# Performance work log

Measured on AMD Instinct MI355X. Metric: run time of the kernel, lower is better.

Reference implementation:

```python
import jax, jax.numpy as jnp
import numpy as np

D_MODEL = 96
D_INNER = 2 * D_MODEL          # expand=2
D_STATE = 16
D_CONV = 4
DT_RANK = 6                    # ceil(96/16)


def setup_inputs() -> dict:
    key = jax.random.key(0)
    ks = jax.random.split(key, 12)
    B, C, H, W = 4, D_MODEL, 64, 64
    # dt_proj bias init (inverse-softplus of dt sampled log-uniform in [1e-3, 1e-1])
    dtv = jnp.exp(jax.random.uniform(ks[7], (D_INNER,), jnp.float32)
                  * (np.log(0.1) - np.log(0.001)) + np.log(0.001))
    dtv = jnp.clip(dtv, 1e-4, None)
    dt_proj_b = dtv + jnp.log(-jnp.expm1(-dtv))
    dt_std = DT_RANK ** -0.5
    return {
        "x": jax.random.normal(ks[0], (B, C, H, W), jnp.float32),
        "proj_w": jax.random.normal(ks[1], (2 * C, C, 1, 1), jnp.float32) * 0.05,
        "dconv_w": jax.random.normal(ks[2], (C, 2 * C, 3, 3), jnp.float32) * 0.02,
        "in_proj_w": jax.random.normal(ks[3], (2 * D_INNER, C), jnp.float32) * 0.05,
        "conv1d_w": jax.random.normal(ks[4], (D_INNER, D_CONV), jnp.float32) * 0.2,
        "conv1d_b": jnp.zeros((D_INNER,), jnp.float32),
        "x_proj_w": jax.random.normal(ks[5], (DT_RANK + 2 * D_STATE, D_INNER), jnp.float32) * 0.05,
        "dt_proj_w": jax.random.uniform(ks[6], (D_INNER, DT_RANK), jnp.float32, -dt_std, dt_std),
        "dt_proj_b": dt_proj_b,
        "A_log": jnp.log(jnp.tile(jnp.arange(1, D_STATE + 1, dtype=jnp.float32), (D_INNER, 1))),
        "D": jnp.ones((D_INNER,), jnp.float32),
        "out_proj_w": jax.random.normal(ks[8], (C, D_INNER), jnp.float32) * 0.05,
    }


def _cssm_forward(x, proj_w, dconv_w, in_proj_w, conv1d_w, conv1d_b,
                  x_proj_w, dt_proj_w, dt_proj_b, A_log, D, out_proj_w):
    Bsz, Cdim, H, W = x.shape
    L = H * W
    # proj (1x1 conv, no bias) then dconv (3x3 conv, pad 1, no bias)
    xp = jax.lax.conv_general_dilated(x, proj_w, (1, 1), 'VALID',
                                      dimension_numbers=('NCHW', 'OIHW', 'NCHW'))
    xp = jax.lax.conv_general_dilated(xp, dconv_w, (1, 1), ((1, 1), (1, 1)),
                                      dimension_numbers=('NCHW', 'OIHW', 'NCHW'))
    seq = xp.reshape(Bsz, Cdim, L).transpose(0, 2, 1)            # (B, L, C)
    # in_proj (no bias) -> (B, 2*d_inner, L)
    xz = jnp.einsum('blc,ec->bel', seq, in_proj_w)
    xin, z = jnp.split(xz, 2, axis=1)                             # (B, d_inner, L) each
    # causal depthwise conv1d (pad d_conv-1 on left) + SiLU
    xpad = jnp.pad(xin, ((0, 0), (0, 0), (D_CONV - 1, 0)))
    xc = jax.lax.conv_general_dilated(xpad, conv1d_w[:, None, :], (1,), 'VALID',
                                      dimension_numbers=('NCH', 'OIH', 'NCH'),
                                      feature_group_count=D_INNER)
    xc = jax.nn.silu(xc + conv1d_b[None, :, None])                # (B, d_inner, L)
    # x_proj -> dt (rank), B (state), C (state)
    x_dbl = jnp.einsum('bdl,ed->ble', xc, x_proj_w)               # (B, L, rank+2n)
    dt, Bc, Cc = jnp.split(x_dbl, [DT_RANK, DT_RANK + D_STATE], axis=-1)
    delta = jax.nn.softplus(jnp.einsum('blr,dr->bld', dt, dt_proj_w) + dt_proj_b)  # (B,L,d)
    A = -jnp.exp(A_log)                                           # (d, n)
    u = xc.transpose(0, 2, 1)                                     # (B, L, d)
    # selective scan: h_t = exp(delta_t A) * h_{t-1} + delta_t B_t u_t  (diag, per channel/state)
    dA = jnp.exp(delta[..., None] * A)                            # (B,L,d,n)
    dBu = delta[..., None] * Bc[:, :, None, :] * u[..., None]     # (B,L,d,n)

    def combine(c1, c2):
        a1, b1 = c1
        a2, b2 = c2
        return a2 * a1, a2 * b1 + b2

    _, h = jax.lax.associative_scan(combine, (dA, dBu), axis=1)   # (B,L,d,n)
    y = jnp.einsum('bldn,bln->bld', h, Cc) + D * u                # (B,L,d)
    y = y * jax.nn.silu(z.transpose(0, 2, 1))                     # gate
    out = jnp.einsum('bld,cd->blc', y, out_proj_w)                # (B,L,C)
    return out.transpose(0, 2, 1).reshape(Bsz, Cdim, H, W)


def reference(x, proj_w, dconv_w, in_proj_w, conv1d_w, conv1d_b,
              x_proj_w, dt_proj_w, dt_proj_b, A_log, D, out_proj_w):
    return _cssm_forward(x, proj_w, dconv_w, in_proj_w, conv1d_w, conv1d_b,
                         x_proj_w, dt_proj_w, dt_proj_b, A_log, D, out_proj_w)
```

## Files before the change

### kernel.cpp

```cpp
#include <hip/hip_runtime.h>
#include <math.h>

#define LL    4096
#define CDIM  96
#define DIN   192
#define NST   16
#define XE    38

typedef __attribute__((ext_vector_type(8))) short v8s;
typedef __attribute__((ext_vector_type(4))) float v4f;
typedef unsigned short ushort_t;
typedef unsigned int uint_t;

#if __has_builtin(__builtin_amdgcn_exp2f)
__device__ __forceinline__ float fexp2(float x) { return __builtin_amdgcn_exp2f(x); }
#else
__device__ __forceinline__ float fexp2(float x) { return exp2f(x); }
#endif
#if __has_builtin(__builtin_amdgcn_logf)
__device__ __forceinline__ float flog2(float x) { return __builtin_amdgcn_logf(x); }
#else
__device__ __forceinline__ float flog2(float x) { return __log2f(x); }
#endif

__device__ __forceinline__ float siluf(float x) {
    return x * __builtin_amdgcn_rcpf(1.f + fexp2(-1.44269504f * x));
}
__device__ __forceinline__ ushort_t f2bf(float f) {
    uint_t u = __builtin_bit_cast(uint_t, f);
    return (ushort_t)((u + 0x7fffu + ((u >> 16) & 1u)) >> 16);
}
__device__ __forceinline__ float bf2f(ushort_t u) {
    return __builtin_bit_cast(float, (uint_t)u << 16);
}

__global__ __launch_bounds__(256) void k_prep(const float* __restrict__ proj_w,
                                              const float* __restrict__ dconv_w,
                                              const float* __restrict__ in_proj_w,
                                              const float* __restrict__ out_proj_w,
                                              const float* __restrict__ x_proj_w,
                                              const float* __restrict__ x,
                                              ushort_t* __restrict__ Wbf,
                                              ushort_t* __restrict__ Wibf,
                                              ushort_t* __restrict__ Wobf,
                                              ushort_t* __restrict__ Wxbf,
                                              ushort_t* __restrict__ xT) {
    int bid = blockIdx.x;
    if (bid < 576) {
        int i = bid * 256 + threadIdx.x;
        if (i < 82944) {
            int k = i % 9;
            int c = (i / 9) % 96;
            int o = i / 864;
            float s = 0.f;
            for (int j = 0; j < 192; ++j)
                s += dconv_w[(o * 192 + j) * 9 + k] * proj_w[j * 96 + c];
            Wbf[(k * 96 + o) * 96 + c] = f2bf(s);
            return;
        }
        i -= 82944;
        if (i < 36864) { Wibf[i] = f2bf(in_proj_w[i]); return; }
        i -= 36864;
        if (i < 18432) { Wobf[i] = f2bf(out_proj_w[i]); return; }
        i -= 18432;
        if (i < 9216) {
            int e = i / 192;
            Wxbf[i] = (e < XE) ? f2bf(x_proj_w[i]) : (ushort_t)0;
        }
        return;
    }
    int bid2 = bid - 576;
    int yy = bid2 % 66;
    int b  = bid2 / 66;
    int yv = yy - 1;
    for (int i = threadIdx.x; i < 68 * 12; i += 256) {
        int xx = i % 68, cig = i / 68;
        int xv = xx - 1;
        ushort_t u[8];
        if (yv >= 0 && yv < 64 && xv >= 0 && xv < 64) {
            const float* sp = x + ((size_t)(b * 96 + cig * 8)) * LL + yv * 64 + xv;
#pragma unroll
            for (int j = 0; j < 8; ++j) u[j] = f2bf(sp[j * LL]);
        } else {
#pragma unroll
            for (int j = 0; j < 8; ++j) u[j] = 0;
        }
        uint4 pk;
        pk.x = u[0] | ((uint_t)u[1] << 16); pk.y = u[2] | ((uint_t)u[3] << 16);
        pk.z = u[4] | ((uint_t)u[5] << 16); pk.w = u[6] | ((uint_t)u[7] << 16);
        *(uint4*)(xT + (((size_t)b * 66 + yy) * 68 + xx) * 96 + cig * 8) = pk;
    }
}

__global__ __launch_bounds__(384, 2) void k_convin(const ushort_t* __restrict__ xT,
                                                   const ushort_t* __restrict__ Wbf,
                                                   const ushort_t* __restrict__ Wibf,
                                                   ushort_t* __restrict__ xzb) {
    __shared__ ushort_t s_seq[32 * 104];
    int tid = threadIdx.x;
    int w = tid >> 6, l = tid & 63;
    int n = l & 15, g = l >> 4;
    int blk = blockIdx.x;
    int b = blk >> 7, rem = blk & 127;
    int y = rem >> 1, half = rem & 1;
    int lx = (w & 1) * 16;
    int x0 = half * 32 + lx;
    int co0 = (w >> 1) * 32;
    v4f acc0 = {0.f, 0.f, 0.f, 0.f};
    v4f acc1 = {0.f, 0.f, 0.f, 0.f};
    const ushort_t* xb = xT + (((size_t)b * 66 + y) * 68 + x0 + n) * 96 + g * 8;
    const ushort_t* aw = Wbf + ((size_t)co0 + n) * 96 + g * 8;
#pragma unroll
    for (int tap = 0; tap < 9; ++tap) {
        int dy = tap / 3, dx = tap % 3;
        const ushort_t* bp = xb + (dy * 68 + dx) * 96;
        const ushort_t* ap = aw + (size_t)tap * 9216;
#pragma unroll
        for (int kk = 0; kk < 3; ++kk) {
            v8s bf = *(const v8s*)(bp + kk * 32);
            v8s a0 = *(const v8s*)(ap + kk * 32);
            v8s a1 = *(const v8s*)(ap + 1536 + kk * 32);
            acc0 = __builtin_amdgcn_mfma_f32_16x16x32_bf16(a0, bf, acc0, 0, 0, 0);
            acc1 = __builtin_amdgcn_mfma_f32_16x16x32_bf16(a1, bf, acc1, 0, 0, 0);
        }
    }
    {
        int ll = lx + n;
        ushort_t* sp = s_seq + ll * 104 + co0 + g * 4;
        ushort4 p0, p1;
        p0.x = f2bf(acc0[0]); p0.y = f2bf(acc0[1]); p0.z = f2bf(acc0[2]); p0.w = f2bf(acc0[3]);
        p1.x = f2bf(acc1[0]); p1.y = f2bf(acc1[1]); p1.z = f2bf(acc1[2]); p1.w = f2bf(acc1[3]);
        *(ushort4*)sp = p0;
        *(ushort4*)(sp + 16) = p1;
    }
    __syncthreads();
    int coh = w * 64;
    v4f acc[4][2];
#pragma unroll
    for (int mt = 0; mt < 4; ++mt)
#pragma unroll
        for (int lt = 0; lt < 2; ++lt) acc[mt][lt] = (v4f){0.f, 0.f, 0.f, 0.f};
    const ushort_t* ap2 = Wibf + ((size_t)coh + n) * 96 + g * 8;
#pragma unroll
    for (int lt = 0; lt < 2; ++lt) {
        const ushort_t* bp2 = s_seq + (lt * 16 + n) * 104 + g * 8;
#pragma unroll
        for (int kk = 0; kk < 3; ++kk) {
            v8s bf = *(const v8s*)(bp2 + kk * 32);
#pragma unroll
            for (int mt = 0; mt < 4; ++mt) {
                v8s af = *(const v8s*)(ap2 + mt * 16 * 96 + kk * 32);
                acc[mt][lt] = __builtin_amdgcn_mfma_f32_16x16x32_bf16(af, bf, acc[mt][lt], 0, 0, 0);
            }
        }
    }
    int l0g = y * 64 + half * 32;
    ushort_t* ob = xzb + (size_t)b * 384 * LL + l0g + n;
#pragma unroll
    for (int mt = 0; mt < 4; ++mt) {
        int e = coh + mt * 16 + g * 4;
#pragma unroll
        for (int lt = 0; lt < 2; ++lt)
#pragma unroll
            for (int r = 0; r < 4; ++r)
                ob[(size_t)(e + r) * LL + lt * 16] = f2bf(acc[mt][lt][r]);
    }
}

__global__ __launch_bounds__(256) void k_conv1d(const ushort_t* __restrict__ xzb,
                                                const float* __restrict__ w,
                                                const float* __restrict__ bias,
                                                float* __restrict__ xc,
                                                ushort_t* __restrict__ xcT) {
    int tid = threadIdx.x;
    int d_l = tid >> 2, tg = tid & 3;
    int b = blockIdx.z, dg = blockIdx.y, tt = blockIdx.x;
    int d = dg * 64 + d_l;
    int t0 = tt * 16 + tg * 4;
    const ushort_t* xin = xzb + (size_t)(b * 384 + d) * LL;
    ushort4 cu = *(const ushort4*)(xin + t0);
    float pm3 = 0.f, pm2 = 0.f, pm1 = 0.f;
    if (t0 > 0) {
        ushort4 pv = *(const ushort4*)(xin + t0 - 4);
        pm3 = bf2f(pv.y); pm2 = bf2f(pv.z); pm1 = bf2f(pv.w);
    }
    float in[7] = {pm3, pm2, pm1, bf2f(cu.x), bf2f(cu.y), bf2f(cu.z), bf2f(cu.w)};
    float w0 = w[d * 4 + 0], w1 = w[d * 4 + 1], w2 = w[d * 4 + 2], w3 = w[d * 4 + 3];
    float bb = bias[d];
    float o[4];
#pragma unroll
    for (int i = 0; i < 4; ++i) {
        float s = bb + w0 * in[i] + w1 * in[i + 1] + w2 * in[i + 2] + w3 * in[i + 3];
        o[i] = siluf(s);
    }
    float4 ov; ov.x = o[0]; ov.y = o[1]; ov.z = o[2]; ov.w = o[3];
    *(float4*)(xc + (size_t)(b * DIN + d) * LL + t0) = ov;
    ushort_t* xt = xcT + ((size_t)b * 4096 + t0) * DIN + d;
#pragma unroll
    for (int i = 0; i < 4; ++i)
        xt[(size_t)i * DIN] = f2bf(o[i]);
}

__global__ __launch_bounds__(256, 4) void k_xprojm(const ushort_t* __restrict__ xcT,
                                                   const ushort_t* __restrict__ Wxbf,
                                                   float* __restrict__ dtT,
                                                   float* __restrict__ BtP,
                                                   float* __restrict__ CtP) {
    int tid = threadIdx.x;
    int w = tid >> 6, l = tid & 63;
    int n = l & 15, g = l >> 4;
    int b = blockIdx.y;
    int l0 = blockIdx.x * 64 + w * 16;
    const ushort_t* bp = xcT + ((size_t)b * 4096 + l0 + n) * 192 + g * 8;
    const ushort_t* ap = Wxbf + (size_t)n * 192 + g * 8;
    v4f acc[3];
#pragma unroll
    for (int m = 0; m < 3; ++m) acc[m] = (v4f){0.f, 0.f, 0.f, 0.f};
#pragma unroll
    for (int kk = 0; kk < 6; ++kk) {
        v8s bf = *(const v8s*)(bp + kk * 32);
#pragma unroll
        for (int m = 0; m < 3; ++m) {
            v8s af = *(const v8s*)(ap + m * 16 * 192 + kk * 32);
            acc[m] = __builtin_amdgcn_mfma_f32_16x16x32_bf16(af, bf, acc[m], 0, 0, 0);
        }
    }
    float* dtb = dtT + (size_t)b * 6 * LL + l0 + n;
    float* Bb = BtP + ((size_t)b * LL + l0 + n) * 16;
    float* Cb = CtP + ((size_t)b * LL + l0 + n) * 16;
#pragma unroll
    for (int m = 0; m < 3; ++m)
#pragma unroll
        for (int r = 0; r < 4; ++r) {
            int e = m * 16 + g * 4 + r;
            float v = acc[m][r];
            if (e < 6)       dtb[(size_t)e * LL] = v;
            else if (e < 22) Bb[e - 6] = v;
            else if (e < 38) Cb[e - 22] = v;
        }
}

__global__ __launch_bounds__(512, 6) void k_scan(const float* __restrict__ dtT,
                                                 const float* __restrict__ dtw,
                                                 const float* __restrict__ dtpb,
                                                 const float* __restrict__ xc,
                                                 const float* __restrict__ BtP,
                                                 const float* __restrict__ CtP,
                                                 const float* __restrict__ A_log,
                                                 const float* __restrict__ Dp,
                                                 ushort_t* __restrict__ xzb) {
    __shared__ float s_d[32 * 132];
    __shared__ float s_u[32 * 132];
    __shared__ float s_a[32][17];
    __shared__ float s_h[32][17];
    int tid = threadIdx.x;
    int n = tid & 15, cg = tid >> 4;
    int bd = blockIdx.x;
    int d = bd % DIN, b = bd / DIN;
    const float* urow = xc + (size_t)(b * DIN + d) * LL;
    const ushort_t* zrow = xzb + (size_t)(b * 384 + DIN + d) * LL;
    ushort_t* ygr = xzb + (size_t)(b * 384 + d) * LL;
    float A2 = -__expf(A_log[d * NST + n]) * 1.44269504f;
    float Dd = Dp[d];

    {
        int t8 = tid * 8;
        int li = ((t8 >> 7) * 132) + (t8 & 127);
        const float* dt0 = dtT + (size_t)b * 6 * LL + t8;
        v4f ra[6], rb[6];
#pragma unroll
        for (int r = 0; r < 6; ++r) {
            ra[r] = *(const v4f*)(dt0 + r * LL);
            rb[r] = *(const v4f*)(dt0 + r * LL + 4);
        }
        const float* wr = dtw + d * 6;
        float w0 = wr[0], w1 = wr[1], w2 = wr[2], w3 = wr[3], w4 = wr[4], w5 = wr[5];
        float bb = dtpb[d];
        v4f spa, spb;
#pragma unroll
        for (int j = 0; j < 4; ++j) {
            float s1 = bb + w0 * ra[0][j] + w1 * ra[1][j] + w2 * ra[2][j]
                          + w3 * ra[3][j] + w4 * ra[4][j] + w5 * ra[5][j];
            spa[j] = 0.69314718f * flog2(1.f + fexp2(s1 * 1.44269504f));
            float s2 = bb + w0 * rb[0][j] + w1 * rb[1][j] + w2 * rb[2][j]
                          + w3 * rb[3][j] + w4 * rb[4][j] + w5 * rb[5][j];
            spb[j] = 0.69314718f * flog2(1.f + fexp2(s2 * 1.44269504f));
        }
        *(v4f*)&s_d[li]     = spa;
        *(v4f*)&s_d[li + 4] = spb;
        *(float4*)&s_u[li]     = *(const float4*)(urow + t8);
        *(float4*)&s_u[li + 4] = *(const float4*)(urow + t8 + 4);
    }
    __syncthreads();

    int t0 = cg * 128;
    int lb = cg * 132;
    const float* pB = BtP + ((size_t)b * LL + t0) * 16 + n;
    const float* pC = CtP + ((size_t)b * LL + t0) * 16 + n;

    float h = 0.f, sdu = 0.f;
    float4 du_c = *(float4*)&s_d[lb];
    float4 u_c  = *(float4*)&s_u[lb];
    float B0 = pB[0], B1 = pB[16], B2 = pB[32], B3 = pB[48];
    for (int s = 0; s < 31; ++s) {
        int ln = lb + s * 4 + 4;
        const float* pBn = pB + s * 64 + 64;
        float4 du_n = *(float4*)&s_d[ln];
        float4 u_n  = *(float4*)&s_u[ln];
        float Bn0 = pBn[0], Bn1 = pBn[16], Bn2 = pBn[32], Bn3 = pBn[48];
        float a0 = fexp2(du_c.x * A2), a1 = fexp2(du_c.y * A2);
        float a2 = fexp2(du_c.z * A2), a3 = fexp2(du_c.w * A2);
        h = fmaf(a0, h, (du_c.x * u_c.x) * B0);
        h = fmaf(a1, h, (du_c.y * u_c.y) * B1);
        h = fmaf(a2, h, (du_c.z * u_c.z) * B2);
        h = fmaf(a3, h, (du_c.w * u_c.w) * B3);
        sdu += (du_c.x + du_c.y) + (du_c.z + du_c.w);
        du_c = du_n; u_c = u_n; B0 = Bn0; B1 = Bn1; B2 = Bn2; B3 = Bn3;
    }
    {
        float a0 = fexp2(du_c.x * A2), a1 = fexp2(du_c.y * A2);
        float a2 = fexp2(du_c.z * A2), a3 = fexp2(du_c.w * A2);
        h = fmaf(a0, h, (du_c.x * u_c.x) * B0);
        h = fmaf(a1, h, (du_c.y * u_c.y) * B1);
        h = fmaf(a2, h, (du_c.z * u_c.z) * B2);
        h = fmaf(a3, h, (du_c.w * u_c.w) * B3);
        sdu += (du_c.x + du_c.y) + (du_c.z + du_c.w);
    }
    s_a[cg][n] = fexp2(sdu * A2);
    s_h[cg][n] = h;
    __syncthreads();

    {
        int l = tid & 63, w = tid >> 6;
        int c = l & 31, nn = (w << 1) | (l >> 5);
        float a  = s_a[c][nn];
        float hh = s_h[c][nn];
#pragma unroll
        for (int st = 1; st < 32; st <<= 1) {
            float ap = __shfl_up(a, st, 32);
            float hp = __shfl_up(hh, st, 32);
            bool ok = (c >= st);
            hh = ok ? fmaf(a, hp, hh) : hh;
            a  = ok ? a * ap : a;
        }
        float h0 = __shfl_up(hh, 1, 32);
        if (c == 0) h0 = 0.f;
        s_a[c][nn] = h0;
    }
    __syncthreads();

    h = s_a[cg][n];
    const int j = n & 3;
    const bool e1 = (j == 1), e2 = (j == 2), e3 = (j == 3);
    du_c = *(float4*)&s_d[lb];
    u_c  = *(float4*)&s_u[lb];
    B0 = pB[0]; B1 = pB[16]; B2 = pB[32]; B3 = pB[48];
    float C0 = pC[0], C1 = pC[16], C2 = pC[32], C3 = pC[48];
    ushort4 z_c = *(const ushort4*)(zrow + t0);
    for (int s = 0; s < 32; ++s) {
        float4 du_n, u_n;
        ushort4 z_n;
        float Bn0, Bn1, Bn2, Bn3, Cn0, Cn1, Cn2, Cn3;
        if (s < 31) {
            int ln = lb + s * 4 + 4;
            const float* pBn = pB + s * 64 + 64;
            const float* pCn = pC + s * 64 + 64;
            du_n = *(float4*)&s_d[ln];
            u_n  = *(float4*)&s_u[ln];
            Bn0 = pBn[0]; Bn1 = pBn[16]; Bn2 = pBn[32]; Bn3 = pBn[48];
            Cn0 = pCn[0]; Cn1 = pCn[16]; Cn2 = pCn[32]; Cn3 = pCn[48];
            z_n = *(const ushort4*)(zrow + t0 + s * 4 + 4);
        }
        float a0 = fexp2(du_c.x * A2), a1 = fexp2(du_c.y * A2);
        float a2 = fexp2(du_c.z * A2), a3 = fexp2(du_c.w * A2);
        h = fmaf(a0, h, (du_c.x * u_c.x) * B0); float p0 = h * C0;
        h = fmaf(a1, h, (du_c.y * u_c.y) * B1); float p1 = h * C1;
        h = fmaf(a2, h, (du_c.z * u_c.z) * B2); float p2 = h * C2;
        h = fmaf(a3, h, (du_c.w * u_c.w) * B3); float p3 = h * C3;
        p0 += __shfl_xor(p0, 1); p0 += __shfl_xor(p0, 2);
        p1 += __shfl_xor(p1, 1); p1 += __shfl_xor(p1, 2);
        p2 += __shfl_xor(p2, 1); p2 += __shfl_xor(p2, 2);
        p3 += __shfl_xor(p3, 1); p3 += __shfl_xor(p3, 2);
        float pj = e3 ? p3 : (e2 ? p2 : (e1 ? p1 : p0));
        pj += __shfl_xor(pj, 4); pj += __shfl_xor(pj, 8);
        float uj = e3 ? u_c.w : (e2 ? u_c.z : (e1 ? u_c.y : u_c.x));
        ushort_t zu = e3 ? z_c.w : (e2 ? z_c.z : (e1 ? z_c.y : z_c.x));
        float yj = fmaf(Dd, uj, pj) * siluf(bf2f(zu));
        if (n < 4)
            ygr[t0 + s * 4 + n] = f2bf(yj);
        du_c = du_n; u_c = u_n; z_c = z_n;
        B0 = Bn0; B1 = Bn1; B2 = Bn2; B3 = Bn3;
        C0 = Cn0; C1 = Cn1; C2 = Cn2; C3 = Cn3;
    }
}

__global__ __launch_bounds__(512, 2) void k_outproj(const ushort_t* __restrict__ xzb,
                                                    const ushort_t* __restrict__ Wobf,
                                                    float* __restrict__ out) {
    __shared__ ushort_t s_yg[64][216];
    int tid = threadIdx.x;
    int b = blockIdx.y;
    int l0 = blockIdx.x * 64;
    const ushort_t* ygb = xzb + (size_t)b * 384 * LL;
    {
        int q = tid & 63, o = tid >> 6;
        if (q < 48) {
            uint4 v[4];
#pragma unroll
            for (int jj = 0; jj < 4; ++jj)
                v[jj] = *(const uint4*)(ygb + (size_t)(q * 4 + jj) * LL + l0 + o * 8);
            const ushort_t* vs = (const ushort_t*)v;
#pragma unroll
            for (int j2 = 0; j2 < 8; ++j2) {
                ushort4 pk;
                pk.x = vs[j2]; pk.y = vs[8 + j2]; pk.z = vs[16 + j2]; pk.w = vs[24 + j2];
                *(ushort4*)&s_yg[o * 8 + j2][q * 4] = pk;
            }
        }
    }
    __syncthreads();
    int w = tid >> 6, l = tid & 63;
    int n = l & 15, g = l >> 4;
    int lt = (w >> 1) * 16;
    int c0 = (w & 1) * 48;
    const ushort_t* bp = &s_yg[lt + n][g * 8];
    const ushort_t* ap = Wobf + ((size_t)c0 + n) * 192 + g * 8;
    v4f acc[3];
#pragma unroll
    for (int m = 0; m < 3; ++m) acc[m] = (v4f){0.f, 0.f, 0.f, 0.f};
#pragma unroll
    for (int kk = 0; kk < 6; ++kk) {
        v8s bf = *(const v8s*)(bp + kk * 32);
#pragma unroll
        for (int m = 0; m < 3; ++m) {
            v8s af = *(const v8s*)(ap + m * 16 * 192 + kk * 32);
            acc[m] = __builtin_amdgcn_mfma_f32_16x16x32_bf16(af, bf, acc[m], 0, 0, 0);
        }
    }
    float* ob = out + (size_t)b * 96 * LL + l0 + lt + n;
#pragma unroll
    for (int m = 0; m < 3; ++m)
#pragma unroll
        for (int r = 0; r < 4; ++r)
            ob[(size_t)(c0 + m * 16 + g * 4 + r) * LL] = acc[m][r];
}

extern "C" void kernel_launch(void* const* d_in, const int* in_sizes, int n_in,
                              void* d_out, int out_size, void* d_ws, size_t ws_size,
                              hipStream_t stream) {
    const float* x         = (const float*)d_in[0];
    const float* proj_w    = (const float*)d_in[1];
    const float* dconv_w   = (const float*)d_in[2];
    const float* in_proj_w = (const float*)d_in[3];
    const float* conv1d_w  = (const float*)d_in[4];
    const float* conv1d_b  = (const float*)d_in[5];
    const float* x_proj_w  = (const float*)d_in[6];
    const float* dt_proj_w = (const float*)d_in[7];
    const float* dt_proj_b = (const float*)d_in[8];
    const float* A_log     = (const float*)d_in[9];
    const float* Dp        = (const float*)d_in[10];
    const float* out_proj_w= (const float*)d_in[11];
    float* out = (float*)d_out;
    float* ws  = (float*)d_ws;

    ushort_t* Wbf  = (ushort_t*)ws;
    ushort_t* Wibf = (ushort_t*)(ws + 41472);
    ushort_t* Wobf = (ushort_t*)(ws + 59904);
    ushort_t* Wxbf = (ushort_t*)(ws + 69120);
    ushort_t* xT   = (ushort_t*)(ws + 73728);
    ushort_t* xzb  = (ushort_t*)(ws + 1721856);
    float* xc   = ws + 4867584;
    float* dtT  = xc + 3145728;
    float* BtP  = dtT + 98304;
    float* CtP  = BtP + 262144;
    ushort_t* xcT = (ushort_t*)(CtP + 262144);

    k_prep<<<dim3(840), dim3(256), 0, stream>>>(proj_w, dconv_w, in_proj_w, out_proj_w,
                                                x_proj_w, x, Wbf, Wibf, Wobf, Wxbf, xT);
    k_convin<<<dim3(512), dim3(384), 0, stream>>>(xT, Wbf, Wibf, xzb);
    k_conv1d<<<dim3(256, 3, 4), dim3(256), 0, stream>>>(xzb, conv1d_w, conv1d_b, xc, xcT);
    k_xprojm<<<dim3(64, 4), dim3(256), 0, stream>>>(xcT, Wxbf, dtT, BtP, CtP);
    k_scan<<<dim3(768), dim3(512), 0, stream>>>(dtT, dt_proj_w, dt_proj_b, xc, BtP, CtP,
                                                A_log, Dp, xzb);
    k_outproj<<<dim3(64, 4), dim3(512), 0, stream>>>(xzb, Wobf, out);
}
```

Measured before the change: 114.9 us.

## Recompute conv1d in scan instead of storing fp32 xc; retile outproj

Drops the fp32 xc buffer that conv1d wrote and the scan read back. The scan now recomputes the depthwise conv1d plus SiLU from the bf16 xin rows, which removes a 12MB write and read of global memory in exchange for a small amount of extra arithmetic. The out-projection kernel is also retiled to 16-position blocks with 384 threads, one MFMA tile per wave, giving more blocks and higher occupancy. The dt load in the scan is split into two halves to lower register pressure.

Result: no change. 115.9 us (+0.9%).

```diff
diff --git a/kernel.cpp b/kernel.cpp
--- a/kernel.cpp
+++ b/kernel.cpp
@@ -170,7 +170,6 @@
 __global__ __launch_bounds__(256) void k_conv1d(const ushort_t* __restrict__ xzb,
                                                 const float* __restrict__ w,
                                                 const float* __restrict__ bias,
-                                                float* __restrict__ xc,
                                                 ushort_t* __restrict__ xcT) {
     int tid = threadIdx.x;
     int d_l = tid >> 2, tg = tid & 3;
@@ -187,18 +186,12 @@
     float in[7] = {pm3, pm2, pm1, bf2f(cu.x), bf2f(cu.y), bf2f(cu.z), bf2f(cu.w)};
     float w0 = w[d * 4 + 0], w1 = w[d * 4 + 1], w2 = w[d * 4 + 2], w3 = w[d * 4 + 3];
     float bb = bias[d];
-    float o[4];
+    ushort_t* xt = xcT + ((size_t)b * 4096 + t0) * DIN + d;
 #pragma unroll
     for (int i = 0; i < 4; ++i) {
         float s = bb + w0 * in[i] + w1 * in[i + 1] + w2 * in[i + 2] + w3 * in[i + 3];
-        o[i] = siluf(s);
-    }
-    float4 ov; ov.x = o[0]; ov.y = o[1]; ov.z = o[2]; ov.w = o[3];
-    *(float4*)(xc + (size_t)(b * DIN + d) * LL + t0) = ov;
-    ushort_t* xt = xcT + ((size_t)b * 4096 + t0) * DIN + d;
-#pragma unroll
-    for (int i = 0; i < 4; ++i)
-        xt[(size_t)i * DIN] = f2bf(o[i]);
+        xt[(size_t)i * DIN] = f2bf(siluf(s));
+    }
 }
 
 __global__ __launch_bounds__(256, 4) void k_xprojm(const ushort_t* __restrict__ xcT,
@@ -243,7 +236,8 @@
 __global__ __launch_bounds__(512, 6) void k_scan(const float* __restrict__ dtT,
                                                  const float* __restrict__ dtw,
                                                  const float* __restrict__ dtpb,
-                                                 const float* __restrict__ xc,
+                                                 const float* __restrict__ c1w,
+                                                 const float* __restrict__ c1b,
                                                  const float* __restrict__ BtP,
                                                  const float* __restrict__ CtP,
                                                  const float* __restrict__ A_log,
@@ -257,7 +251,7 @@
     int n = tid & 15, cg = tid >> 4;
     int bd = blockIdx.x;
     int d = bd % DIN, b = bd / DIN;
-    const float* urow = xc + (size_t)(b * DIN + d) * LL;
+    const ushort_t* xin  = xzb + (size_t)(b * 384 + d) * LL;
     const ushort_t* zrow = xzb + (size_t)(b * 384 + DIN + d) * LL;
     ushort_t* ygr = xzb + (size_t)(b * 384 + d) * LL;
     float A2 = -__expf(A_log[d * NST + n]) * 1.44269504f;
@@ -266,30 +260,53 @@
     {
         int t8 = tid * 8;
         int li = ((t8 >> 7) * 132) + (t8 & 127);
+        float ee[11];
+        if (t8 > 0) {
+            ushort4 pv = *(const ushort4*)(xin + t8 - 4);
+            ee[0] = bf2f(pv.y); ee[1] = bf2f(pv.z); ee[2] = bf2f(pv.w);
+        } else {
+            ee[0] = ee[1] = ee[2] = 0.f;
+        }
+        v8s cu = *(const v8s*)(xin + t8);
+#pragma unroll
+        for (int j = 0; j < 8; ++j) ee[3 + j] = bf2f((ushort_t)cu[j]);
+        float cw0 = c1w[d * 4], cw1 = c1w[d * 4 + 1], cw2 = c1w[d * 4 + 2], cw3 = c1w[d * 4 + 3];
+        float cb = c1b[d];
+#pragma unroll
+        for (int j = 0; j < 8; ++j) {
+            float s = cb + cw0 * ee[j] + cw1 * ee[j + 1] + cw2 * ee[j + 2] + cw3 * ee[j + 3];
+            s_u[li + j] = siluf(s);
+        }
         const float* dt0 = dtT + (size_t)b * 6 * LL + t8;
-        v4f ra[6], rb[6];
-#pragma unroll
-        for (int r = 0; r < 6; ++r) {
-            ra[r] = *(const v4f*)(dt0 + r * LL);
-            rb[r] = *(const v4f*)(dt0 + r * LL + 4);
-        }
         const float* wr = dtw + d * 6;
         float w0 = wr[0], w1 = wr[1], w2 = wr[2], w3 = wr[3], w4 = wr[4], w5 = wr[5];
         float bb = dtpb[d];
-        v4f spa, spb;
-#pragma unroll
-        for (int j = 0; j < 4; ++j) {
-            float s1 = bb + w0 * ra[0][j] + w1 * ra[1][j] + w2 * ra[2][j]
-                          + w3 * ra[3][j] + w4 * ra[4][j] + w5 * ra[5][j];
-            spa[j] = 0.69314718f * flog2(1.f + fexp2(s1 * 1.44269504f));
-            float s2 = bb + w0 * rb[0][j] + w1 * rb[1][j] + w2 * rb[2][j]
-                          + w3 * rb[3][j] + w4 * rb[4][j] + w5 * rb[5][j];
-            spb[j] = 0.69314718f * flog2(1.f + fexp2(s2 * 1.44269504f));
-        }
-        *(v4f*)&s_d[li]     = spa;
-        *(v4f*)&s_d[li + 4] = spb;
-        *(float4*)&s_u[li]     = *(const float4*)(urow + t8);
-        *(float4*)&s_u[li + 4] = *(const float4*)(urow + t8 + 4);
+        {
+            v4f ra[6];
+#pragma unroll
+            for (int r = 0; r < 6; ++r) ra[r] = *(const v4f*)(dt0 + r * LL);
+            v4f spa;
+#pragma unroll
+            for (int j = 0; j < 4; ++j) {
+                float s1 = bb + w0 * ra[0][j] + w1 * ra[1][j] + w2 * ra[2][j]
+                              + w3 * ra[3][j] + w4 * ra[4][j] + w5 * ra[5][j];
+                spa[j] = 0.69314718f * flog2(1.f + fexp2(s1 * 1.44269504f));
+            }
+            *(v4f*)&s_d[li] = spa;
+        }
+        {
+            v4f rb[6];
+#pragma unroll
+            for (int r = 0; r < 6; ++r) rb[r] = *(const v4f*)(dt0 + r * LL + 4);
+            v4f spb;
+#pragma unroll
+            for (int j = 0; j < 4; ++j) {
+                float s2 = bb + w0 * rb[0][j] + w1 * rb[1][j] + w2 * rb[2][j]
+                              + w3 * rb[3][j] + w4 * rb[4][j] + w5 * rb[5][j];
+                spb[j] = 0.69314718f * flog2(1.f + fexp2(s2 * 1.44269504f));
+            }
+            *(v4f*)&s_d[li + 4] = spb;
+        }
     }
     __syncthreads();
 
@@ -394,55 +411,45 @@
     }
 }
 
-__global__ __launch_bounds__(512, 2) void k_outproj(const ushort_t* __restrict__ xzb,
+__global__ __launch_bounds__(384, 6) void k_outproj(const ushort_t* __restrict__ xzb,
                                                     const ushort_t* __restrict__ Wobf,
                                                     float* __restrict__ out) {
-    __shared__ ushort_t s_yg[64][216];
+    __shared__ ushort_t s_yg[16][232];
     int tid = threadIdx.x;
     int b = blockIdx.y;
-    int l0 = blockIdx.x * 64;
+    int l0 = blockIdx.x * 16;
     const ushort_t* ygb = xzb + (size_t)b * 384 * LL;
-    {
-        int q = tid & 63, o = tid >> 6;
-        if (q < 48) {
-            uint4 v[4];
-#pragma unroll
-            for (int jj = 0; jj < 4; ++jj)
-                v[jj] = *(const uint4*)(ygb + (size_t)(q * 4 + jj) * LL + l0 + o * 8);
-            const ushort_t* vs = (const ushort_t*)v;
-#pragma unroll
-            for (int j2 = 0; j2 < 8; ++j2) {
-                ushort4 pk;
-                pk.x = vs[j2]; pk.y = vs[8 + j2]; pk.z = vs[16 + j2]; pk.w = vs[24 + j2];
-                *(ushort4*)&s_yg[o * 8 + j2][q * 4] = pk;
-            }
+    if (tid < 96) {
+        int q = tid >> 1, o = tid & 1;
+        uint4 v[4];
+#pragma unroll
+        for (int jj = 0; jj < 4; ++jj)
+            v[jj] = *(const uint4*)(ygb + (size_t)(q * 4 + jj) * LL + l0 + o * 8);
+        const ushort_t* vs = (const ushort_t*)v;
+#pragma unroll
+        for (int j2 = 0; j2 < 8; ++j2) {
+            ushort4 pk;
+            pk.x = vs[j2]; pk.y = vs[8 + j2]; pk.z = vs[16 + j2]; pk.w = vs[24 + j2];
+            *(ushort4*)&s_yg[o * 8 + j2][q * 4] = pk;
         }
     }
     __syncthreads();
     int w = tid >> 6, l = tid & 63;
     int n = l & 15, g = l >> 4;
-    int lt = (w >> 1) * 16;
-    int c0 = (w & 1) * 48;
-    const ushort_t* bp = &s_yg[lt + n][g * 8];
+    int c0 = w * 16;
+    const ushort_t* bp = &s_yg[n][g * 8];
     const ushort_t* ap = Wobf + ((size_t)c0 + n) * 192 + g * 8;
-    v4f acc[3];
-#pragma unroll
-    for (int m = 0; m < 3; ++m) acc[m] = (v4f){0.f, 0.f, 0.f, 0.f};
+    v4f acc = {0.f, 0.f, 0.f, 0.f};
 #pragma unroll
     for (int kk = 0; kk < 6; ++kk) {
         v8s bf = *(const v8s*)(bp + kk * 32);
-#pragma unroll
-        for (int m = 0; m < 3; ++m) {
-            v8s af = *(const v8s*)(ap + m * 16 * 192 + kk * 32);
-            acc[m] = __builtin_amdgcn_mfma_f32_16x16x32_bf16(af, bf, acc[m], 0, 0, 0);
-        }
-    }
-    float* ob = out + (size_t)b * 96 * LL + l0 + lt + n;
-#pragma unroll
-    for (int m = 0; m < 3; ++m)
-#pragma unroll
-        for (int r = 0; r < 4; ++r)
-            ob[(size_t)(c0 + m * 16 + g * 4 + r) * LL] = acc[m][r];
+        v8s af = *(const v8s*)(ap + kk * 32);
+        acc = __builtin_amdgcn_mfma_f32_16x16x32_bf16(af, bf, acc, 0, 0, 0);
+    }
+    float* ob = out + (size_t)b * 96 * LL + l0 + n;
+#pragma unroll
+    for (int r = 0; r < 4; ++r)
+        ob[(size_t)(c0 + g * 4 + r) * LL] = acc[r];
 }
 
 extern "C" void kernel_launch(void* const* d_in, const int* in_sizes, int n_in,
@@ -469,8 +476,7 @@
     ushort_t* Wxbf = (ushort_t*)(ws + 69120);
     ushort_t* xT   = (ushort_t*)(ws + 73728);
     ushort_t* xzb  = (ushort_t*)(ws + 1721856);
-    float* xc   = ws + 4867584;
-    float* dtT  = xc + 3145728;
+    float* dtT  = ws + 4867584;
     float* BtP  = dtT + 98304;
     float* CtP  = BtP + 262144;
     ushort_t* xcT = (ushort_t*)(CtP + 262144);
@@ -478,9 +484,10 @@
     k_prep<<<dim3(840), dim3(256), 0, stream>>>(proj_w, dconv_w, in_proj_w, out_proj_w,
                                                 x_proj_w, x, Wbf, Wibf, Wobf, Wxbf, xT);
     k_convin<<<dim3(512), dim3(384), 0, stream>>>(xT, Wbf, Wibf, xzb);
-    k_conv1d<<<dim3(256, 3, 4), dim3(256), 0, stream>>>(xzb, conv1d_w, conv1d_b, xc, xcT);
+    k_conv1d<<<dim3(256, 3, 4), dim3(256), 0, stream>>>(xzb, conv1d_w, conv1d_b, xcT);
     k_xprojm<<<dim3(64, 4), dim3(256), 0, stream>>>(xcT, Wxbf, dtT, BtP, CtP);
-    k_scan<<<dim3(768), dim3(512), 0, stream>>>(dtT, dt_proj_w, dt_proj_b, xc, BtP, CtP,
+    k_scan<<<dim3(768), dim3(512), 0, stream>>>(dtT, dt_proj_w, dt_proj_b,
+                                                conv1d_w, conv1d_b, BtP, CtP,
                                                 A_log, Dp, xzb);
-    k_outproj<<<dim3(64, 4), dim3(512), 0, stream>>>(xzb, Wobf, out);
-}
+    k_outproj<<<dim3(256, 4), dim3(384), 0, stream>>>(xzb, Wobf, out);
+}
```
